# Performance work log

Hardware: AMD Instinct MI355X
Metric: run time of the kernel (lower is better)

Reference implementation:

```python
import jax, jax.numpy as jnp
import numpy as np

HEADS, DIM, N = 16, 128, 2048
NEG = -1e9


def setup_inputs() -> dict:
    key = jax.random.key(0)
    ks = jax.random.split(key, 8)
    xavier = lambda k, shape, fan: jax.random.uniform(
        k, shape, jnp.float32, -1.0, 1.0) * np.sqrt(6.0 / fan)
    return {
        "q": jax.random.normal(ks[0], (N, DIM), jnp.float32),
        "k": jax.random.normal(ks[1], (N, DIM), jnp.float32),
        "v": jax.random.normal(ks[2], (N, DIM), jnp.float32),
        "mask": jax.random.randint(ks[3], (N, N), 0, 2) > 0,
        "Q": xavier(ks[4], (HEADS, DIM, DIM), 2 * DIM),
        "K": xavier(ks[5], (HEADS, DIM, DIM), 2 * DIM),
        "V": xavier(ks[6], (HEADS, DIM, DIM), 2 * DIM),
        "last": xavier(ks[7], (HEADS * DIM, DIM), HEADS * DIM + DIM),
    }


def reference(q, k, v, Q, K, V, last, mask):
    # per-head projections: [n, d] x [h, d, d] -> [h, n, d]
    qp = jnp.einsum('nd,hde->hne', q, Q)
    kp = jnp.einsum('nd,hde->hne', k, K)
    vp = jnp.einsum('nd,hde->hne', v, V)
    n = qp.shape[1]
    # NOTE: original computes k @ q^T and scales by sqrt(seq_len) (q.size(1) after projection)
    att = jnp.einsum('hid,hjd->hij', kp, qp)  # [h, n, n]
    fmask = mask.astype(jnp.float32)
    att = att * fmask / jnp.sqrt(jnp.float32(n)) + NEG * (1.0 - fmask)
    att = jax.nn.softmax(att, axis=2)
    out = jnp.einsum('hij,hjd->hid', att, vp)            # [h, n, d]
    out = jnp.transpose(out, (1, 0, 2)).reshape(n, -1)   # n (heads d)
    return out @ last
```

## Files before the change

kernel.cpp:

```cpp
#include <hip/hip_runtime.h>
#include <hip/hip_bf16.h>


#define HN 16
#define NN 2048
#define DD 128

typedef __attribute__((ext_vector_type(8))) short short8;
typedef __attribute__((ext_vector_type(4))) short short4v;
typedef __attribute__((ext_vector_type(4))) float float4v;
typedef __attribute__((ext_vector_type(16))) float f32x16;
typedef __attribute__((ext_vector_type(4))) unsigned int uint4v;

#define CROW(r) ((((r) & 3)) + 8 * ((r) >> 2))

__device__ inline unsigned short f2bf(float f) {
    unsigned int u = __builtin_bit_cast(unsigned int, f);
    unsigned int r = (u + 0x7fffu + ((u >> 16) & 1u)) >> 16;
    return (unsigned short)r;
}

__device__ inline unsigned int cvtpk(float lo, float hi) {
    unsigned int w;
    asm("v_cvt_pk_bf16_f32 %0, %1, %2" : "=v"(w) : "v"(lo), "v"(hi));
    return w;
}

__device__ inline void plswap(unsigned int& x, unsigned int& y) {
#if __has_builtin(__builtin_amdgcn_permlane32_swap)
    typedef int int2v __attribute__((ext_vector_type(2)));
    int2v r = __builtin_amdgcn_permlane32_swap((int)x, (int)y, false, false);
    x = (unsigned int)r[0];
    y = (unsigned int)r[1];
#else
    const unsigned int sx = (unsigned int)__shfl_xor((int)x, 32);
    const unsigned int sy = (unsigned int)__shfl_xor((int)y, 32);
    const bool hiHalf = (threadIdx.x & 32) != 0;
    const unsigned int nx = hiHalf ? sy : x;
    const unsigned int ny = hiHalf ? y : sx;
    x = nx; y = ny;
#endif
}

__device__ inline short8 ld_bf8(const float* __restrict__ p) {
    const float4v a = *(const float4v*)p;
    const float4v b = *(const float4v*)(p + 4);
    short8 r;
    r[0] = (short)f2bf(a[0]); r[1] = (short)f2bf(a[1]);
    r[2] = (short)f2bf(a[2]); r[3] = (short)f2bf(a[3]);
    r[4] = (short)f2bf(b[0]); r[5] = (short)f2bf(b[1]);
    r[6] = (short)f2bf(b[2]); r[7] = (short)f2bf(b[3]);
    return r;
}

__device__ inline short8 ld2x4(const unsigned short* p) {
    const short4v lo = *(const short4v*)p;
    const short4v hi = *(const short4v*)(p + 4);
    short8 r;
    r[0] = lo[0]; r[1] = lo[1]; r[2] = lo[2]; r[3] = lo[3];
    r[4] = hi[0]; r[5] = hi[1]; r[6] = hi[2]; r[7] = hi[3];
    return r;
}

__global__ void sentinel_kernel(float* out, int n) {
    int i = blockIdx.x * 256 + threadIdx.x;
    if (i < n) out[i] = 2.0f;
}

__global__ __launch_bounds__(256) void prep_kernel(
    const int* __restrict__ mask,
    unsigned long long* __restrict__ mbT,
    float* __restrict__ out, int out_n,
    const float* __restrict__ Qw,
    const float* __restrict__ Kw,
    const float* __restrict__ Vw,
    unsigned short* __restrict__ wsW)
{
    __shared__ __align__(16) unsigned short Wt[128 * 132];
    const int bx = blockIdx.x;
    const int tid = threadIdx.x;

    if (bx < 4096) {
        const int wgrp = bx * 4 + (tid >> 6);
        const int lane = tid & 63;
        const int word0 = wgrp * 4;
        const int i = word0 >> 5;
        const int w = word0 & 31;
        const int* row = mask + (size_t)i * NN + w * 64;
        unsigned long long b[4];
#pragma unroll
        for (int c = 0; c < 4; c++)
            b[c] = __ballot(row[c * 64 + lane] != 0);
        if (lane == 0) {
#pragma unroll
            for (int c = 0; c < 4; c++) mbT[(size_t)(w + c) * NN + i] = b[c];
        }
        const int z = bx * 256 + tid;
        if (z < out_n) out[z] = 0.f;
    } else {
        const int idx = bx - 4096;
        const int h = idx & 15, t = idx >> 4;
        const float* W = ((t == 0) ? Qw : ((t == 1) ? Kw : Vw)) + h * DD * DD;
        unsigned short* o = wsW + ((size_t)t * HN + h) * DD * DD;

        for (int idx2 = tid * 2; idx2 < DD * DD; idx2 += 512) {
            const int d = idx2 >> 7, e = idx2 & 127;
            const float2 w2 = *(const float2*)(W + idx2);
            Wt[(e + 0) * 132 + d] = f2bf(w2.x);
            Wt[(e + 1) * 132 + d] = f2bf(w2.y);
        }
        __syncthreads();
        for (int idx8 = tid * 8; idx8 < DD * DD; idx8 += 2048) {
            const int e = idx8 >> 7, d = idx8 & 127;
            *(short8*)(o + idx8) = ld2x4(&Wt[e * 132 + d]);
        }
    }
}

__global__ __launch_bounds__(256) void proj4_kernel(
    const float* __restrict__ q,
    const float* __restrict__ k,
    const float* __restrict__ v,
    const unsigned short* __restrict__ wsW,
    unsigned short* __restrict__ ws)
{
    __shared__ __align__(16) unsigned short Wt[128 * 136];
    const int t = blockIdx.z, h = blockIdx.y, cb = blockIdx.x;
    const int tid = threadIdx.x;
    const float* in = (t == 0) ? q : ((t == 1) ? k : v);
    const unsigned short* WTg = wsW + ((size_t)t * HN + h) * DD * DD;
    unsigned short* out = ws + (size_t)t * (HN * NN * DD) + (size_t)h * (NN * DD);

#pragma unroll
    for (int it = 0; it < 8; it++) {
        const int idx8 = tid * 8 + it * 2048;
        const int row = idx8 >> 7, col = idx8 & 127;
        *(short8*)(&Wt[row * 136 + col]) = *(const short8*)(WTg + idx8);
    }
    __syncthreads();

    const int wave = tid >> 6, lane = tid & 63;
    const int quad = lane >> 4, l16 = lane & 15;

#pragma unroll 1
    for (int rt = 0; rt < 2; rt++) {
        const int row0 = cb * 128 + rt * 64 + wave * 16;

        float4v acc[8];
#pragma unroll
        for (int c = 0; c < 8; c++) acc[c] = {0.f, 0.f, 0.f, 0.f};

        if (t < 2) {
#pragma unroll
            for (int kk = 0; kk < 4; kk++) {
                const short8 a = ld_bf8(in + (size_t)(row0 + l16) * DD + kk * 32 + quad * 8);
#pragma unroll
                for (int c = 0; c < 8; c++) {
                    const short8 b = *(const short8*)(&Wt[(c * 16 + l16) * 136 + kk * 32 + quad * 8]);
                    acc[c] = __builtin_amdgcn_mfma_f32_16x16x32_bf16(a, b, acc[c], 0, 0, 0);
                }
            }
            if (t == 0) {
#pragma unroll
                for (int c = 0; c < 8; c++)
#pragma unroll
                    for (int r = 0; r < 4; r++) {
                        const int row = row0 + quad * 4 + r;
                        out[(size_t)(((row >> 5) * 8 + c)) * 512 + (row & 31) * 16 + l16]
                            = f2bf(acc[c][r]);
                    }
            } else {
#pragma unroll
                for (int c = 0; c < 8; c++)
#pragma unroll
                    for (int r = 0; r < 4; r++)
                        out[(size_t)(row0 + quad * 4 + r) * DD + c * 16 + l16] = f2bf(acc[c][r]);
            }
        } else {
#pragma unroll
            for (int kk = 0; kk < 4; kk++) {
                const short8 bv = ld_bf8(in + (size_t)(row0 + l16) * DD + kk * 32 + quad * 8);
#pragma unroll
                for (int c = 0; c < 8; c++) {
                    const short8 aw = *(const short8*)(&Wt[(c * 16 + l16) * 136 + kk * 32 + quad * 8]);
                    acc[c] = __builtin_amdgcn_mfma_f32_16x16x32_bf16(aw, bv, acc[c], 0, 0, 0);
                }
            }
#pragma unroll
            for (int c = 0; c < 8; c++)
#pragma unroll
                for (int r = 0; r < 4; r++) {
                    const int d = c * 16 + quad * 4 + r;
                    out[(size_t)(row0 >> 4) * 2048 + d * 16 + l16] = f2bf(acc[c][r]);
                }
        }
    }
}

__global__ __launch_bounds__(256, 2) void attn_kernel(
    unsigned short* __restrict__ ws,
    const unsigned long long* __restrict__ mbT)
{
    __shared__ __align__(16) float obuf[8192];
    __shared__ float lbuf[192];

    const int bid = blockIdx.x;
    const int xcd = bid & 7;
    const int h  = xcd + 8 * (bid >> 8);
    const int ib = (bid >> 3) & 31;
    const int tid = threadIdx.x;
    const int wave = tid >> 6, lane = tid & 63;
    const int ig = wave >> 1;
    const int h2 = wave & 1;
    const int l31 = lane & 31;
    const int hi = lane >> 5;

    const unsigned short* qA  = ws + (size_t)h * (NN * DD);
    const unsigned short* kp  = ws + (size_t)(HN * NN * DD) + (size_t)h * (NN * DD);
    const unsigned short* vpB = ws + (size_t)(2 * HN * NN * DD) + (size_t)h * (NN * DD);
    unsigned short* ao = ws + (size_t)(3 * HN * NN * DD);

    const int i0 = ib * 64;
    const float scale = 0.022097086912079612f;

    short8 kpf[8];
    {
        const int row = i0 + ig * 32 + l31;
#pragma unroll
        for (int kk = 0; kk < 8; kk++)
            kpf[kk] = *(const short8*)(kp + (size_t)row * DD + kk * 16 + hi * 8);
    }

    const unsigned short* qbase = qA + l31 * 16 + hi * 8;
    const unsigned short* vbase = vpB + l31 * 16 + hi * 8;

    f32x16 o[4];
#pragma unroll
    for (int dt = 0; dt < 4; dt++)
#pragma unroll
        for (int r = 0; r < 16; r++) o[dt][r] = 0.f;
    float lacc = 0.f;

    short8 qfA[8], qfB[8];

#define QLD(QF, JT) do {                                                        \
        const unsigned short* p_ = qbase + (size_t)(((JT) * 2 + h2) * 8) * 512; \
        _Pragma("unroll")                                                       \
        for (int kk = 0; kk < 8; kk++)                                          \
            QF[kk] = *(const short8*)(p_ + kk * 512);                           \
    } while (0)

    auto COMPUTE = [&](const short8 (&qf)[8], int jt) {
        short8 vf[8];
#pragma unroll
        for (int ks = 0; ks < 2; ks++)
#pragma unroll
            for (int dt = 0; dt < 4; dt++)
                vf[ks * 4 + dt] = *(const short8*)(vbase
                    + (size_t)(jt * 4 + h2 * 2 + ks) * 2048 + dt * 512);
        const unsigned long long mrow = mbT[(size_t)jt * NN + i0 + ig * 32 + l31];
        const unsigned int m2 = (unsigned int)(mrow >> (h2 * 32 + hi * 4));

        f32x16 s;
#pragma unroll
        for (int r = 0; r < 16; r++) s[r] = 0.f;
        __builtin_amdgcn_s_setprio(1);
#pragma unroll
        for (int kk = 0; kk < 8; kk++)
            s = __builtin_amdgcn_mfma_f32_32x32x16_bf16(qf[kk], kpf[kk], s, 0, 0, 0);
        __builtin_amdgcn_s_setprio(0);

#pragma unroll
        for (int r = 0; r < 16; r++) {
            const float x = ((m2 >> CROW(r)) & 1u) ? fmaf(s[r], scale, -5.0f) : -50.0f;
            s[r] = __expf(x);
        }
        float ls = (((s[0] + s[1]) + (s[2] + s[3])) + ((s[4] + s[5]) + (s[6] + s[7])))
                 + (((s[8] + s[9]) + (s[10] + s[11])) + ((s[12] + s[13]) + (s[14] + s[15])));
        ls += __shfl_xor(ls, 32);
        lacc += ls;

        short8 pa[2];
#pragma unroll
        for (int ks = 0; ks < 2; ks++) {
            const int b = ks * 8;
            unsigned int x0 = cvtpk(s[b + 0], s[b + 1]);
            unsigned int y0 = cvtpk(s[b + 4], s[b + 5]);
            unsigned int x1 = cvtpk(s[b + 2], s[b + 3]);
            unsigned int y1 = cvtpk(s[b + 6], s[b + 7]);
            plswap(x0, y0);
            plswap(x1, y1);
            uint4v w; w[0] = x0; w[1] = x1; w[2] = y0; w[3] = y1;
            pa[ks] = __builtin_bit_cast(short8, w);
        }

        __builtin_amdgcn_s_setprio(1);
#pragma unroll
        for (int ks = 0; ks < 2; ks++)
#pragma unroll
            for (int dt = 0; dt < 4; dt++)
                o[dt] = __builtin_amdgcn_mfma_f32_32x32x16_bf16(pa[ks], vf[ks * 4 + dt], o[dt], 0, 0, 0);
        __builtin_amdgcn_s_setprio(0);
    };

    QLD(qfA, 0);
#pragma unroll 1
    for (int jt = 0; jt < 32; jt += 2) {
        QLD(qfB, jt + 1);
        COMPUTE(qfA, jt);
        if (jt + 2 < 32) QLD(qfA, jt + 2);
        COMPUTE(qfB, jt + 1);
    }
#undef QLD

    if (h2 == 1) {
#pragma unroll
        for (int dt = 0; dt < 4; dt++)
#pragma unroll
            for (int r = 0; r < 16; r++)
                obuf[(((ig * 2 + hi) * 4 + dt) * 16 + r) * 32 + l31] = o[dt][r];
        if (hi == 0) lbuf[ig * 32 + l31] = lacc;
    }
    __syncthreads();
    if (h2 == 0) {
        const float lt = lacc + lbuf[ig * 32 + l31];
        const float inv = (lt > 0.f) ? (1.0f / lt) : 0.f;
        if (hi == 0) lbuf[64 + ig * 32 + l31] = inv;
#pragma unroll
        for (int dt = 0; dt < 4; dt++)
#pragma unroll
            for (int r = 0; r < 16; r++) {
                const int row = CROW(r) + hi * 4;
                const float val = (o[dt][r] + obuf[(((ig * 2 + hi) * 4 + dt) * 16 + r) * 32 + l31])
                                  * lbuf[64 + ig * 32 + row];
                ao[(size_t)(i0 + ig * 32 + row) * (HN * DD) + h * DD + dt * 32 + l31] = f2bf(val);
            }
    }
}

__global__ __launch_bounds__(256) void final3_kernel(
    const unsigned short* __restrict__ ao,
    const float* __restrict__ last,
    float* __restrict__ outp)
{
    __shared__ __align__(16) unsigned short lt[32 * 260];
    const int tid = threadIdx.x;
    const int wave = tid >> 6, lane = tid & 63;
    const int quad = lane >> 4, l16 = lane & 15;
    const int i0 = blockIdx.x * 64;
    const int e0 = blockIdx.y * 32;
    const int k0 = blockIdx.z * 256;

#pragma unroll
    for (int idx2 = tid * 2; idx2 < 256 * 32; idx2 += 512) {
        const int kk = idx2 >> 5, e = idx2 & 31;
        const float2 w2 = *(const float2*)(last + (size_t)(k0 + kk) * DD + e0 + e);
        lt[(e + 0) * 260 + kk] = f2bf(w2.x);
        lt[(e + 1) * 260 + kk] = f2bf(w2.y);
    }
    __syncthreads();

    float4v acc[2];
    acc[0] = {0.f, 0.f, 0.f, 0.f};
    acc[1] = {0.f, 0.f, 0.f, 0.f};

    const unsigned short* arow = ao + (size_t)(i0 + wave * 16 + l16) * (HN * DD) + k0;

#pragma unroll
    for (int kb = 0; kb < 4; kb++) {
#pragma unroll
        for (int ks = 0; ks < 2; ks++) {
            const short8 a = *(const short8*)(arow + kb * 64 + ks * 32 + quad * 8);
#pragma unroll
            for (int dc = 0; dc < 2; dc++) {
                const short8 b = ld2x4(&lt[(dc * 16 + l16) * 260 + kb * 64 + ks * 32 + quad * 8]);
                acc[dc] = __builtin_amdgcn_mfma_f32_16x16x32_bf16(a, b, acc[dc], 0, 0, 0);
            }
        }
    }

#pragma unroll
    for (int r = 0; r < 4; r++)
#pragma unroll
        for (int dc = 0; dc < 2; dc++)
            atomicAdd(&outp[(size_t)(i0 + wave * 16 + quad * 4 + r) * DD + e0 + dc * 16 + l16],
                      acc[dc][r]);
}

extern "C" void kernel_launch(void* const* d_in, const int* in_sizes, int n_in,
                              void* d_out, int out_size, void* d_ws, size_t ws_size,
                              hipStream_t stream)
{
    const float* q    = (const float*)d_in[0];
    const float* k    = (const float*)d_in[1];
    const float* v    = (const float*)d_in[2];
    const int*   mask = (const int*)d_in[3];
    const float* Qw   = (const float*)d_in[4];
    const float* Kw   = (const float*)d_in[5];
    const float* Vw   = (const float*)d_in[6];
    const float* last = (const float*)d_in[7];
    unsigned short* ws  = (unsigned short*)d_ws;
    float* out = (float*)d_out;

    const size_t shorts_main = (size_t)4 * HN * NN * DD;
    const size_t mb_bytes = (size_t)NN * (NN / 64) * 8;
    const size_t needed = shorts_main * sizeof(unsigned short) + mb_bytes;
    if (ws_size < needed) {
        sentinel_kernel<<<(out_size + 255) / 256, 256, 0, stream>>>(out, out_size);
        return;
    }
    unsigned long long* mbT = (unsigned long long*)(ws + shorts_main);
    unsigned short* wsW = ws + (size_t)3 * HN * NN * DD;

    prep_kernel<<<dim3(4096 + 48), 256, 0, stream>>>(mask, mbT, out, out_size,
                                                     Qw, Kw, Vw, wsW);
    proj4_kernel<<<dim3(16, 16, 3), 256, 0, stream>>>(q, k, v, wsW, ws);
    attn_kernel<<<dim3(512), 256, 0, stream>>>(ws, mbT);
    final3_kernel<<<dim3(32, 4, 8), 256, 0, stream>>>(ws + (size_t)3 * HN * NN * DD, last, out);
}
```

Before: 160.0 us.

## Fuse output projection into attention kernel epilogue with atomic accumulation

```diff
diff --git a/kernel.cpp b/kernel.cpp
--- a/kernel.cpp
+++ b/kernel.cpp
@@ -199,9 +199,12 @@
 
 __global__ __launch_bounds__(256, 2) void attn_kernel(
     unsigned short* __restrict__ ws,
-    const unsigned long long* __restrict__ mbT)
+    const unsigned long long* __restrict__ mbT,
+    const float* __restrict__ last,
+    float* __restrict__ outp)
 {
-    __shared__ __align__(16) float obuf[8192];
+    __shared__ __align__(16) float obuf[2 * 128 * 33];
+    __shared__ __align__(16) unsigned short lastT[128 * 132];
     __shared__ float lbuf[192];
 
     const int bid = blockIdx.x;
@@ -218,10 +221,19 @@
     const unsigned short* qA  = ws + (size_t)h * (NN * DD);
     const unsigned short* kp  = ws + (size_t)(HN * NN * DD) + (size_t)h * (NN * DD);
     const unsigned short* vpB = ws + (size_t)(2 * HN * NN * DD) + (size_t)h * (NN * DD);
-    unsigned short* ao = ws + (size_t)(3 * HN * NN * DD);
 
     const int i0 = ib * 64;
     const float scale = 0.022097086912079612f;
+
+    {
+        const float* lastH = last + (size_t)h * DD * DD;
+        for (int idx2 = tid * 2; idx2 < DD * DD; idx2 += 512) {
+            const int kk = idx2 >> 7, e = idx2 & 127;
+            const float2 w2 = *(const float2*)(lastH + idx2);
+            lastT[(e + 0) * 132 + kk] = f2bf(w2.x);
+            lastT[(e + 1) * 132 + kk] = f2bf(w2.y);
+        }
+    }
 
     short8 kpf[8];
     {
@@ -318,10 +330,11 @@
         for (int dt = 0; dt < 4; dt++)
 #pragma unroll
             for (int r = 0; r < 16; r++)
-                obuf[(((ig * 2 + hi) * 4 + dt) * 16 + r) * 32 + l31] = o[dt][r];
+                obuf[(size_t)(ig * 128 + dt * 32 + l31) * 33 + CROW(r) + hi * 4] = o[dt][r];
         if (hi == 0) lbuf[ig * 32 + l31] = lacc;
     }
     __syncthreads();
+
     if (h2 == 0) {
         const float lt = lacc + lbuf[ig * 32 + l31];
         const float inv = (lt > 0.f) ? (1.0f / lt) : 0.f;
@@ -331,60 +344,44 @@
 #pragma unroll
             for (int r = 0; r < 16; r++) {
                 const int row = CROW(r) + hi * 4;
-                const float val = (o[dt][r] + obuf[(((ig * 2 + hi) * 4 + dt) * 16 + r) * 32 + l31])
-                                  * lbuf[64 + ig * 32 + row];
-                ao[(size_t)(i0 + ig * 32 + row) * (HN * DD) + h * DD + dt * 32 + l31] = f2bf(val);
+                const size_t oi = (size_t)(ig * 128 + dt * 32 + l31) * 33 + row;
+                obuf[oi] = (o[dt][r] + obuf[oi]) * lbuf[64 + ig * 32 + row];
             }
     }
-}
-
-__global__ __launch_bounds__(256) void final3_kernel(
-    const unsigned short* __restrict__ ao,
-    const float* __restrict__ last,
-    float* __restrict__ outp)
-{
-    __shared__ __align__(16) unsigned short lt[32 * 260];
-    const int tid = threadIdx.x;
-    const int wave = tid >> 6, lane = tid & 63;
-    const int quad = lane >> 4, l16 = lane & 15;
-    const int i0 = blockIdx.x * 64;
-    const int e0 = blockIdx.y * 32;
-    const int k0 = blockIdx.z * 256;
-
-#pragma unroll
-    for (int idx2 = tid * 2; idx2 < 256 * 32; idx2 += 512) {
-        const int kk = idx2 >> 5, e = idx2 & 31;
-        const float2 w2 = *(const float2*)(last + (size_t)(k0 + kk) * DD + e0 + e);
-        lt[(e + 0) * 260 + kk] = f2bf(w2.x);
-        lt[(e + 1) * 260 + kk] = f2bf(w2.y);
-    }
     __syncthreads();
 
-    float4v acc[2];
-    acc[0] = {0.f, 0.f, 0.f, 0.f};
-    acc[1] = {0.f, 0.f, 0.f, 0.f};
-
-    const unsigned short* arow = ao + (size_t)(i0 + wave * 16 + l16) * (HN * DD) + k0;
-
-#pragma unroll
-    for (int kb = 0; kb < 4; kb++) {
-#pragma unroll
-        for (int ks = 0; ks < 2; ks++) {
-            const short8 a = *(const short8*)(arow + kb * 64 + ks * 32 + quad * 8);
-#pragma unroll
-            for (int dc = 0; dc < 2; dc++) {
-                const short8 b = ld2x4(&lt[(dc * 16 + l16) * 260 + kb * 64 + ks * 32 + quad * 8]);
-                acc[dc] = __builtin_amdgcn_mfma_f32_16x16x32_bf16(a, b, acc[dc], 0, 0, 0);
-            }
-        }
-    }
-
-#pragma unroll
-    for (int r = 0; r < 4; r++)
-#pragma unroll
-        for (int dc = 0; dc < 2; dc++)
-            atomicAdd(&outp[(size_t)(i0 + wave * 16 + quad * 4 + r) * DD + e0 + dc * 16 + l16],
-                      acc[dc][r]);
+    short8 af[8];
+#pragma unroll
+    for (int kk = 0; kk < 8; kk++) {
+        const float* ob = &obuf[(size_t)(ig * 128 + kk * 16 + hi * 8) * 33 + l31];
+        uint4v w;
+        w[0] = cvtpk(ob[0 * 33], ob[1 * 33]);
+        w[1] = cvtpk(ob[2 * 33], ob[3 * 33]);
+        w[2] = cvtpk(ob[4 * 33], ob[5 * 33]);
+        w[3] = cvtpk(ob[6 * 33], ob[7 * 33]);
+        af[kk] = __builtin_bit_cast(short8, w);
+    }
+    f32x16 acc2[2];
+#pragma unroll
+    for (int ebx = 0; ebx < 2; ebx++)
+#pragma unroll
+        for (int r = 0; r < 16; r++) acc2[ebx][r] = 0.f;
+#pragma unroll
+    for (int kk = 0; kk < 8; kk++) {
+#pragma unroll
+        for (int ebx = 0; ebx < 2; ebx++) {
+            const short8 bf = ld2x4(&lastT[(size_t)((h2 * 2 + ebx) * 32 + l31) * 132
+                                           + kk * 16 + hi * 8]);
+            acc2[ebx] = __builtin_amdgcn_mfma_f32_32x32x16_bf16(af[kk], bf, acc2[ebx], 0, 0, 0);
+        }
+    }
+#pragma unroll
+    for (int ebx = 0; ebx < 2; ebx++)
+#pragma unroll
+        for (int r = 0; r < 16; r++)
+            atomicAdd(&outp[(size_t)(i0 + ig * 32 + CROW(r) + 4 * hi) * DD
+                            + (h2 * 2 + ebx) * 32 + l31],
+                      acc2[ebx][r]);
 }
 
 extern "C" void kernel_launch(void* const* d_in, const int* in_sizes, int n_in,
@@ -415,6 +412,5 @@
     prep_kernel<<<dim3(4096 + 48), 256, 0, stream>>>(mask, mbT, out, out_size,
                                                      Qw, Kw, Vw, wsW);
     proj4_kernel<<<dim3(16, 16, 3), 256, 0, stream>>>(q, k, v, wsW, ws);
-    attn_kernel<<<dim3(512), 256, 0, stream>>>(ws, mbT);
-    final3_kernel<<<dim3(32, 4, 8), 256, 0, stream>>>(ws + (size_t)3 * HN * NN * DD, last, out);
-}
+    attn_kernel<<<dim3(512), 256, 0, stream>>>(ws, mbT, last, out);
+}
```

Result: faster. 156.3 us (-2.3%).
